# Kernel optimization log

Hardware: AMD Instinct MI355X
Metric: run time of the kernel (lower is better)

## Reference

```python
import jax, jax.numpy as jnp
import numpy as np

NUM_GROUPS = 32
EPS = 1e-6


def group_norm(x, gamma, beta):
    # x: [b, c, h, w]
    b, c, h, w = x.shape
    g = NUM_GROUPS
    xg = x.reshape(b, g, c // g, h, w)
    mean = jnp.mean(xg, axis=(2, 3, 4), keepdims=True)
    var = jnp.var(xg, axis=(2, 3, 4), keepdims=True)
    xg = (xg - mean) * jax.lax.rsqrt(var + EPS)
    x = xg.reshape(b, c, h, w)
    return x * gamma[None, :, None, None] + beta[None, :, None, None]


def conv1x1(x, w, bias):
    # x: [b, c_in, h, w], w: [c_out, c_in], bias: [c_out]
    return jnp.einsum('bihw,oi->bohw', x, w) + bias[None, :, None, None]


def setup_inputs() -> dict:
    key = jax.random.key(0)
    ks = jax.random.split(key, 10)
    c = 512
    b, h, w = 4, 64, 64
    scale = 1.0 / np.sqrt(c)
    inp = {
        'x': jax.random.normal(ks[0], (b, c, h, w), dtype=jnp.float32),
        'gn_gamma': jnp.ones((c,), dtype=jnp.float32),
        'gn_beta': jnp.zeros((c,), dtype=jnp.float32),
        'wq': jax.random.normal(ks[1], (c, c), dtype=jnp.float32) * scale,
        'bq': jnp.zeros((c,), dtype=jnp.float32),
        'wk': jax.random.normal(ks[2], (c, c), dtype=jnp.float32) * scale,
        'bk': jnp.zeros((c,), dtype=jnp.float32),
        'wv': jax.random.normal(ks[3], (c, c), dtype=jnp.float32) * scale,
        'bv': jnp.zeros((c,), dtype=jnp.float32),
        'wo': jax.random.normal(ks[4], (c, c), dtype=jnp.float32) * scale,
        'bo': jnp.zeros((c,), dtype=jnp.float32),
    }
    return inp


def reference(x, gn_gamma, gn_beta, wq, bq, wk, bk, wv, bv, wo, bo):
    b, c, h, w = x.shape
    h_ = group_norm(x, gn_gamma, gn_beta)
    q = conv1x1(h_, wq, bq)
    k = conv1x1(h_, wk, bk)
    v = conv1x1(h_, wv, bv)
    n = h * w
    q = q.reshape(b, c, n).transpose(0, 2, 1)  # [b, n, c]
    k = k.reshape(b, c, n)                      # [b, c, n]
    v = v.reshape(b, c, n).transpose(0, 2, 1)  # [b, n, c]
    sim = jnp.einsum('bqc,bck->bqk', q, k) * (c ** -0.5)  # [b, n, n]
    attn = jax.nn.softmax(sim, axis=-1)
    out = jnp.einsum('bqk,bkc->bqc', attn, v)  # [b, n, c]
    out = out.transpose(0, 2, 1).reshape(b, c, h, w)
    out = conv1x1(out, wo, bo)
    return x + out
```

## Files before the change

kernel.cpp:

```cpp
#include <hip/hip_runtime.h>


typedef __attribute__((ext_vector_type(8))) short bf16x8;
typedef __attribute__((ext_vector_type(4))) float f32x4;

#define MFMA16(a, b, c) __builtin_amdgcn_mfma_f32_16x16x32_bf16((a), (b), (c), 0, 0, 0)

#define B_   4
#define C_   512
#define N_   4096
#define SCALE 0.044194173824159216f
#define ESHIFT 12.0f

__device__ __forceinline__ unsigned short f2bf(float f) {
    union { float f; unsigned int u; } v; v.f = f;
    unsigned int r = (v.u + 0x7fffu + ((v.u >> 16) & 1u)) >> 16;
    return (unsigned short)r;
}
__device__ __forceinline__ float bf2f(unsigned short s) {
    union { unsigned int u; float f; } v; v.u = ((unsigned int)s) << 16;
    return v.f;
}

__device__ __forceinline__ void async16(const unsigned short* g, unsigned short* l) {
    __builtin_amdgcn_global_load_lds((const __attribute__((address_space(1))) unsigned int*)g,
                                     (__attribute__((address_space(3))) unsigned int*)l,
                                     16, 0, 0);
}

__global__ __launch_bounds__(256) void gn_partial(const float* __restrict__ x,
                                                  float* __restrict__ part) {
    int blk = blockIdx.x;
    int gid = blk >> 2, qtr = blk & 3;
    const float4* base = (const float4*)(x + (size_t)gid * 65536) + qtr * 4096;
    float s = 0.f, ss = 0.f;
    for (int i = threadIdx.x; i < 4096; i += 256) {
        float4 v = base[i];
        s  += v.x + v.y + v.z + v.w;
        ss += v.x * v.x + v.y * v.y + v.z * v.z + v.w * v.w;
    }
    __shared__ float red[512];
    int t = threadIdx.x;
    red[t] = s; red[256 + t] = ss;
    __syncthreads();
    for (int st = 128; st > 0; st >>= 1) {
        if (t < st) { red[t] += red[t + st]; red[256 + t] += red[256 + t + st]; }
        __syncthreads();
    }
    if (t == 0) { part[blk] = red[0]; part[512 + blk] = red[256]; }
}

__global__ __launch_bounds__(256) void gn_apply(const float* __restrict__ x,
                                                const float* __restrict__ gamma,
                                                const float* __restrict__ beta,
                                                const float* __restrict__ part,
                                                unsigned short* __restrict__ ht) {
    __shared__ float tile[64][65];
    __shared__ float mrs[4][2];
    int j0 = blockIdx.x * 64, c0 = blockIdx.y * 64, b = blockIdx.z;
    int t = threadIdx.x;
    if (t < 4) {
        int gid = b * 32 + (c0 >> 4) + t;
        float s = 0.f, ss = 0.f;
#pragma unroll
        for (int q = 0; q < 4; ++q) { s += part[gid * 4 + q]; ss += part[512 + gid * 4 + q]; }
        float mean = s * (1.f / 65536.f);
        float var  = ss * (1.f / 65536.f) - mean * mean;
        mrs[t][0] = mean;
        mrs[t][1] = rsqrtf(var + 1e-6f);
    }
    __syncthreads();
#pragma unroll
    for (int i = 0; i < 16; ++i) {
        int lid = i * 256 + t;
        int cl = lid >> 6, jl = lid & 63;
        int c = c0 + cl;
        float v = x[((size_t)b * C_ + c) * N_ + j0 + jl];
        tile[cl][jl] = (v - mrs[cl >> 4][0]) * mrs[cl >> 4][1] * gamma[c] + beta[c];
    }
    __syncthreads();
#pragma unroll
    for (int i = 0; i < 16; ++i) {
        int lid = i * 256 + t;
        int jl = lid >> 6, cl = lid & 63;
        ht[((size_t)b * N_ + j0 + jl) * C_ + c0 + cl] = f2bf(tile[cl][jl]);
    }
}

__global__ __launch_bounds__(256) void wconv(const float* __restrict__ wq,
                                             const float* __restrict__ wk,
                                             const float* __restrict__ wv,
                                             const float* __restrict__ wo,
                                             unsigned short* __restrict__ dst) {
    size_t i = (size_t)blockIdx.x * 256 + threadIdx.x;
    int m = (int)(i >> 18);
    size_t off = i & 262143;
    const float* src = (m == 0) ? wq : (m == 1) ? wk : (m == 2) ? wv : wo;
    dst[i] = f2bf(src[off]);
}

template <typename EPI>
__device__ __forceinline__ void gemm_core(const unsigned short* __restrict__ Abase,
                                          const unsigned short* __restrict__ Bbase,
                                          size_t lda, size_t ldb, int K, EPI epi) {
    __shared__ unsigned short hl[2][128 * 64];
    __shared__ unsigned short wl[2][128 * 64];
    int t = threadIdx.x;
    int wv = t >> 6, lane = t & 63, l15 = lane & 15, quad = lane >> 4;
    int wm = wv & 1, wn = wv >> 1;
    int srow = lane >> 3;
    int sch  = ((lane & 7) ^ srow) * 8;
    int xr = l15 & 7;
    f32x4 acc[4][4] = {};
#pragma unroll
    for (int i = 0; i < 4; ++i) {
        int seg = wv * 4 + i;
        size_t row = seg * 8 + srow;
        async16(&Abase[row * lda + sch], &hl[0][seg * 512]);
        async16(&Bbase[row * ldb + sch], &wl[0][seg * 512]);
    }
    int nk = K >> 6;
    for (int k = 0; k < nk; ++k) {
        int cur = k & 1;
        __builtin_amdgcn_s_waitcnt(0x3F70);
        __syncthreads();
        if (k + 1 < nk) {
            int k0 = (k + 1) << 6;
#pragma unroll
            for (int i = 0; i < 4; ++i) {
                int seg = wv * 4 + i;
                size_t row = seg * 8 + srow;
                async16(&Abase[row * lda + k0 + sch], &hl[cur ^ 1][seg * 512]);
                async16(&Bbase[row * ldb + k0 + sch], &wl[cur ^ 1][seg * 512]);
            }
        }
#pragma unroll
        for (int kk = 0; kk < 2; ++kk) {
            int sl = (((kk << 2) + quad) ^ xr) * 8;
            bf16x8 af[4], bfr[4];
#pragma unroll
            for (int mi = 0; mi < 4; ++mi)
                af[mi] = *(const bf16x8*)&hl[cur][(wm * 64 + mi * 16 + l15) * 64 + sl];
#pragma unroll
            for (int ni = 0; ni < 4; ++ni)
                bfr[ni] = *(const bf16x8*)&wl[cur][(wn * 64 + ni * 16 + l15) * 64 + sl];
#pragma unroll
            for (int mi = 0; mi < 4; ++mi)
#pragma unroll
                for (int ni = 0; ni < 4; ++ni)
                    acc[mi][ni] = MFMA16(af[mi], bfr[ni], acc[mi][ni]);
        }
    }
    epi(acc, wm, wn, l15, quad);
}

__global__ __launch_bounds__(256) void gemm_qkv(const unsigned short* __restrict__ Ht,
                                                const unsigned short* __restrict__ Wb,
                                                const float* __restrict__ bq,
                                                const float* __restrict__ bk,
                                                const float* __restrict__ bv,
                                                unsigned short* __restrict__ Qt,
                                                unsigned short* __restrict__ Kt,
                                                unsigned short* __restrict__ Vg) {
    int b = blockIdx.z, j0 = blockIdx.x * 128;
    int ct = blockIdx.y;
    int slab = ct >> 2, co0 = (ct & 3) * 128;
    const unsigned short* A = Ht + ((size_t)b * N_ + j0) * C_;
    const unsigned short* B = Wb + (size_t)slab * C_ * C_ + (size_t)co0 * C_;
    const float* bias = (slab == 0) ? bq : (slab == 1) ? bk : bv;
    unsigned short* outqk = (slab == 0) ? Qt : Kt;
    gemm_core(A, B, C_, C_, C_,
        [&](f32x4 (&acc)[4][4], int wm, int wn, int l15, int quad) {
        if (slab < 2) {
#pragma unroll
            for (int mi = 0; mi < 4; ++mi)
#pragma unroll
                for (int ni = 0; ni < 4; ++ni)
#pragma unroll
                    for (int r = 0; r < 4; ++r) {
                        int mrow = wm * 64 + mi * 16 + quad * 4 + r;
                        int ncol = wn * 64 + ni * 16 + l15;
                        outqk[((size_t)b * N_ + j0 + mrow) * C_ + co0 + ncol] =
                            f2bf(acc[mi][ni][r] + bias[co0 + ncol]);
                    }
        } else {
#pragma unroll
            for (int mi = 0; mi < 4; ++mi)
#pragma unroll
                for (int ni = 0; ni < 4; ++ni) {
                    int ncol = wn * 64 + ni * 16 + l15;
                    float bb = bias[co0 + ncol];
                    ushort4 pk;
                    pk.x = f2bf(acc[mi][ni][0] + bb);
                    pk.y = f2bf(acc[mi][ni][1] + bb);
                    pk.z = f2bf(acc[mi][ni][2] + bb);
                    pk.w = f2bf(acc[mi][ni][3] + bb);
                    int jb = j0 + wm * 64 + mi * 16 + quad * 4;
                    *(ushort4*)&Vg[((size_t)b * C_ + co0 + ncol) * N_ + jb] = pk;
                }
        }
    });
}

__global__ __launch_bounds__(256) void gemm_qk_exp(const unsigned short* __restrict__ Qt,
                                                   const unsigned short* __restrict__ Kt,
                                                   unsigned short* __restrict__ P,
                                                   float* __restrict__ psum) {
    int b = blockIdx.z, j0 = blockIdx.x * 128, ktile = blockIdx.y;
    int kc0 = ktile * 128;
    const unsigned short* A = Qt + ((size_t)b * N_ + j0) * C_;
    const unsigned short* B = Kt + ((size_t)b * N_ + kc0) * C_;
    gemm_core(A, B, C_, C_, C_,
        [&](f32x4 (&acc)[4][4], int wm, int wn, int l15, int quad) {
        float rs[4][4];
#pragma unroll
        for (int mi = 0; mi < 4; ++mi)
#pragma unroll
            for (int r = 0; r < 4; ++r) rs[mi][r] = 0.f;
#pragma unroll
        for (int mi = 0; mi < 4; ++mi)
#pragma unroll
            for (int ni = 0; ni < 4; ++ni)
#pragma unroll
                for (int r = 0; r < 4; ++r) {
                    int mrow = wm * 64 + mi * 16 + quad * 4 + r;
                    int ncol = wn * 64 + ni * 16 + l15;
                    float p = __expf(acc[mi][ni][r] * SCALE - ESHIFT);
                    rs[mi][r] += p;
                    P[((size_t)b * N_ + j0 + mrow) * N_ + kc0 + ncol] = f2bf(p);
                }
#pragma unroll
        for (int mi = 0; mi < 4; ++mi)
#pragma unroll
            for (int r = 0; r < 4; ++r) {
                float v = rs[mi][r];
                v += __shfl_xor(v, 1);
                v += __shfl_xor(v, 2);
                v += __shfl_xor(v, 4);
                v += __shfl_xor(v, 8);
                if (l15 == 0)
                    psum[(size_t)(wn * 32 + ktile) * 16384 +
                         (size_t)b * N_ + j0 + wm * 64 + mi * 16 + quad * 4 + r] = v;
            }
    });
}

__global__ __launch_bounds__(256) void gemm_pv(const unsigned short* __restrict__ P,
                                               const unsigned short* __restrict__ Vg,
                                               const float* __restrict__ psum,
                                               unsigned short* __restrict__ ao) {
    __shared__ float linv[128];
    int flat = blockIdx.x;
    int xcd = flat & 7, rr = flat >> 3;
    int ct = rr & 3, g = (rr >> 2) * 8 + xcd;
    int b = g & 3, qtile = g >> 2;
    int j0 = qtile * 128, co0 = ct * 128;
    int t = threadIdx.x;
    if (t < 128) {
        size_t q = (size_t)b * N_ + j0 + t;
        float s = 0.f;
#pragma unroll
        for (int i = 0; i < 64; ++i) s += psum[(size_t)i * 16384 + q];
        linv[t] = 1.f / s;
    }
    const unsigned short* A = P + ((size_t)b * N_ + j0) * N_;
    const unsigned short* B = Vg + ((size_t)b * C_ + co0) * N_;
    gemm_core(A, B, N_, N_, N_,
        [&](f32x4 (&acc)[4][4], int wm, int wn, int l15, int quad) {
#pragma unroll
        for (int mi = 0; mi < 4; ++mi)
#pragma unroll
            for (int ni = 0; ni < 4; ++ni)
#pragma unroll
                for (int r = 0; r < 4; ++r) {
                    int mrow = wm * 64 + mi * 16 + quad * 4 + r;
                    int ncol = wn * 64 + ni * 16 + l15;
                    ao[((size_t)b * N_ + j0 + mrow) * C_ + co0 + ncol] =
                        f2bf(acc[mi][ni][r] * linv[mrow]);
                }
    });
}

__global__ __launch_bounds__(256) void gemm_resid(const unsigned short* __restrict__ AObf,
                                                  const unsigned short* __restrict__ Wo,
                                                  const float* __restrict__ bo,
                                                  const float* __restrict__ xres,
                                                  float* __restrict__ out) {
    int b = blockIdx.z, j0 = blockIdx.x * 128, co0 = blockIdx.y * 128;
    const unsigned short* A = AObf + ((size_t)b * N_ + j0) * C_;
    const unsigned short* B = Wo + (size_t)co0 * C_;
    gemm_core(A, B, C_, C_, C_,
        [&](f32x4 (&acc)[4][4], int wm, int wn, int l15, int quad) {
#pragma unroll
        for (int mi = 0; mi < 4; ++mi)
#pragma unroll
            for (int ni = 0; ni < 4; ++ni) {
                int ncol = wn * 64 + ni * 16 + l15;
                int jb = j0 + wm * 64 + mi * 16 + quad * 4;
                size_t o = ((size_t)b * C_ + co0 + ncol) * N_ + jb;
                float bb = bo[co0 + ncol];
                float4 xr = *(const float4*)&xres[o];
                float4 ov;
                ov.x = acc[mi][ni][0] + bb + xr.x;
                ov.y = acc[mi][ni][1] + bb + xr.y;
                ov.z = acc[mi][ni][2] + bb + xr.z;
                ov.w = acc[mi][ni][3] + bb + xr.w;
                *(float4*)&out[o] = ov;
            }
    });
}

__global__ __launch_bounds__(256, 1) void flash_attn(const unsigned short* __restrict__ Qt,
                                                     const unsigned short* __restrict__ Kt,
                                                     const unsigned short* __restrict__ Vg,
                                                     unsigned short* __restrict__ part,
                                                     float* __restrict__ lbuf,
                                                     int nsplit) {
    extern __shared__ unsigned short smem[];
    unsigned short* Kl = smem;
    unsigned short* Vl = smem + 32768;
    unsigned short* Pl = smem + 65536;

    int flat = blockIdx.x;
    int qblk, b, s;
    if (nsplit == 2) { s = flat & 1; b = (flat >> 1) & 3; qblk = flat >> 3; }
    else             { s = 0;        b = flat & 3;        qblk = flat >> 2; }
    int q0 = qblk * 128;
    int t = threadIdx.x, w = t >> 6, lane = t & 63, l15 = lane & 15, quad = lane >> 4;
    int klen = N_ / nsplit, kbeg = s * klen, nkt = klen / 32;
    int xr = l15 & 7;

    const unsigned short* Kbase = Kt + (size_t)b * N_ * C_;
    const unsigned short* Vbase = Vg + (size_t)b * C_ * N_;

    bf16x8 qa[2][16];
#pragma unroll
    for (int u = 0; u < 2; ++u) {
        const unsigned short* qb =
            Qt + ((size_t)b * N_ + q0 + w * 32 + u * 16 + l15) * C_ + quad * 8;
#pragma unroll
        for (int ck = 0; ck < 16; ++ck) qa[u][ck] = *(const bf16x8*)(qb + ck * 32);
    }

    f32x4 o[2][32] = {};
    float lrow[2][4] = {};

    {
        int k0 = kbeg;
#pragma unroll
        for (int i = 0; i < 8; ++i) {
            int r = w * 8 + i;
            async16(Kbase + (size_t)(k0 + r) * C_ + ((lane ^ (r & 7)) * 8), Kl + r * 512);
        }
#pragma unroll
        for (int i = 0; i < 8; ++i) {
            int idx = w * 8 + i, kc = idx >> 3, cb = idx & 7;
            async16(Vbase + (size_t)(cb * 64 + lane) * N_ + k0 + kc * 8,
                    Vl + (kc * 512 + cb * 64) * 8);
        }
    }

    for (int kt = 0; kt < nkt; ++kt) {
        int cur = kt & 1, nxt = cur ^ 1;
        __builtin_amdgcn_s_waitcnt(0x3F70);
        __syncthreads();
        if (kt + 1 < nkt) {
            int k0 = kbeg + (kt + 1) * 32;
#pragma unroll
            for (int i = 0; i < 8; ++i) {
                int r = w * 8 + i;
                async16(Kbase + (size_t)(k0 + r) * C_ + ((lane ^ (r & 7)) * 8),
                        Kl + nxt * 16384 + r * 512);
            }
#pragma unroll
            for (int i = 0; i < 8; ++i) {
                int idx = w * 8 + i, kc = idx >> 3, cb = idx & 7;
                async16(Vbase + (size_t)(cb * 64 + lane) * N_ + k0 + kc * 8,
                        Vl + nxt * 16384 + (kc * 512 + cb * 64) * 8);
            }
        }
        const unsigned short* Kc = Kl + cur * 16384;
        f32x4 s00 = {}, s01 = {}, s10 = {}, s11 = {};
#pragma unroll
        for (int ck = 0; ck < 16; ++ck) {
            int slot = (ck * 4 + quad) ^ xr;
            bf16x8 b0 = *(const bf16x8*)&Kc[l15 * 512 + slot * 8];
            bf16x8 b1 = *(const bf16x8*)&Kc[(16 + l15) * 512 + slot * 8];
            s00 = MFMA16(qa[0][ck], b0, s00);
            s10 = MFMA16(qa[1][ck], b0, s10);
            s01 = MFMA16(qa[0][ck], b1, s01);
            s11 = MFMA16(qa[1][ck], b1, s11);
        }
        unsigned short* pb = &Pl[w * 1152];
#pragma unroll
        for (int r = 0; r < 4; ++r) {
            float p00 = __expf(s00[r] * SCALE - ESHIFT);
            float p01 = __expf(s01[r] * SCALE - ESHIFT);
            float p10 = __expf(s10[r] * SCALE - ESHIFT);
            float p11 = __expf(s11[r] * SCALE - ESHIFT);
            lrow[0][r] += p00 + p01;
            lrow[1][r] += p10 + p11;
            int row0 = (quad * 4 + r) * 36;
            int row1 = (16 + quad * 4 + r) * 36;
            pb[row0 + l15]      = f2bf(p00);
            pb[row0 + 16 + l15] = f2bf(p01);
            pb[row1 + l15]      = f2bf(p10);
            pb[row1 + 16 + l15] = f2bf(p11);
        }
        __builtin_amdgcn_s_waitcnt(0xC07F);
        bf16x8 pa0 = *(const bf16x8*)&Pl[w * 1152 + l15 * 36 + quad * 8];
        bf16x8 pa1 = *(const bf16x8*)&Pl[w * 1152 + (16 + l15) * 36 + quad * 8];
        const unsigned short* Vc = Vl + cur * 16384;
#pragma unroll
        for (int cf = 0; cf < 32; ++cf) {
            bf16x8 vb = *(const bf16x8*)&Vc[(quad * 512 + cf * 16 + l15) * 8];
            o[0][cf] = MFMA16(pa0, vb, o[0][cf]);
            o[1][cf] = MFMA16(pa1, vb, o[1][cf]);
        }
    }
#pragma unroll
    for (int u = 0; u < 2; ++u)
#pragma unroll
        for (int r = 0; r < 4; ++r) {
            float l = lrow[u][r];
            l += __shfl_xor(l, 1);
            l += __shfl_xor(l, 2);
            l += __shfl_xor(l, 4);
            l += __shfl_xor(l, 8);
            lrow[u][r] = l;
        }
    size_t pbase = (size_t)(s * B_ + b) * N_;
#pragma unroll
    for (int u = 0; u < 2; ++u)
#pragma unroll
        for (int cf = 0; cf < 32; ++cf)
#pragma unroll
            for (int r = 0; r < 4; ++r) {
                int q = q0 + w * 32 + u * 16 + quad * 4 + r;
                part[(pbase + q) * C_ + cf * 16 + l15] = f2bf(o[u][cf][r]);
            }
    if (l15 == 0) {
#pragma unroll
        for (int u = 0; u < 2; ++u)
#pragma unroll
            for (int r = 0; r < 4; ++r) {
                int q = q0 + w * 32 + u * 16 + quad * 4 + r;
                lbuf[pbase + q] = lrow[u][r];
            }
    }
}

__global__ __launch_bounds__(256) void attn_combine(const unsigned short* __restrict__ part,
                                                    const float* __restrict__ lbuf,
                                                    unsigned short* __restrict__ ao,
                                                    int nsplit) {
    size_t idx = (size_t)blockIdx.x * 256 + threadIdx.x;
    int cu = (int)(idx & 63);
    size_t row = idx >> 6;
    float l = lbuf[row];
    union { uint4 v; unsigned short u[8]; } p1, p2, outv;
    p1.v = *(const uint4*)&part[row * C_ + cu * 8];
    if (nsplit == 2) {
        l += lbuf[(size_t)B_ * N_ + row];
        p2.v = *(const uint4*)&part[((size_t)B_ * N_ + row) * C_ + cu * 8];
    } else {
        p2.v = make_uint4(0, 0, 0, 0);
    }
    float inv = 1.f / l;
#pragma unroll
    for (int j = 0; j < 8; ++j)
        outv.u[j] = f2bf((bf2f(p1.u[j]) + bf2f(p2.u[j])) * inv);
    *(uint4*)&ao[row * C_ + cu * 8] = outv.v;
}

extern "C" void kernel_launch(void* const* d_in, const int* in_sizes, int n_in,
                              void* d_out, int out_size, void* d_ws, size_t ws_size,
                              hipStream_t stream) {
    const float* x   = (const float*)d_in[0];
    const float* gam = (const float*)d_in[1];
    const float* bet = (const float*)d_in[2];
    const float* wq  = (const float*)d_in[3];
    const float* bq  = (const float*)d_in[4];
    const float* wk  = (const float*)d_in[5];
    const float* bk  = (const float*)d_in[6];
    const float* wv  = (const float*)d_in[7];
    const float* bv  = (const float*)d_in[8];
    const float* wo  = (const float*)d_in[9];
    const float* bo  = (const float*)d_in[10];
    float* out = (float*)d_out;

    char* ws = (char*)d_ws;
    const size_t SZH = (size_t)B_ * N_ * C_ * 2;
    const size_t OFF_HT = 4096;
    const size_t OFF_QT = OFF_HT + SZH;
    const size_t OFF_KT = OFF_QT + SZH;
    const size_t OFF_VG = OFF_KT + SZH;
    const size_t OFF_WB = OFF_VG + SZH;
    const size_t OFF_X  = OFF_WB + 2097152;
    float*          part0 = (float*)ws;
    unsigned short* Ht    = (unsigned short*)(ws + OFF_HT);
    unsigned short* Qt    = (unsigned short*)(ws + OFF_QT);
    unsigned short* Kt    = (unsigned short*)(ws + OFF_KT);
    unsigned short* Vg    = (unsigned short*)(ws + OFF_VG);
    unsigned short* Wb    = (unsigned short*)(ws + OFF_WB);
    unsigned short* AObf  = Ht;

    const size_t SZPSUM = 64ull * 16384 * 4;
    const size_t SZP    = (size_t)B_ * N_ * N_ * 2;
    float*          psum = (float*)(ws + OFF_X);
    unsigned short* P    = (unsigned short*)(ws + OFF_X + SZPSUM);
    size_t needA = OFF_X + SZPSUM + SZP;

    float*          lbuf = (float*)(ws + OFF_X);
    unsigned short* partb = (unsigned short*)(ws + OFF_X + 262144);
    size_t needB2 = OFF_X + 262144 + 2 * SZH;

    gn_partial<<<512, 256, 0, stream>>>(x, part0);
    gn_apply<<<dim3(64, 8, B_), 256, 0, stream>>>(x, gam, bet, part0, Ht);
    wconv<<<4096, 256, 0, stream>>>(wq, wk, wv, wo, Wb);
    gemm_qkv<<<dim3(32, 12, B_), 256, 0, stream>>>(Ht, Wb, bq, bk, bv, Qt, Kt, Vg);

    if (ws_size >= needA) {
        gemm_qk_exp<<<dim3(32, 32, B_), 256, 0, stream>>>(Qt, Kt, P, psum);
        gemm_pv<<<512, 256, 0, stream>>>(P, Vg, psum, AObf);
    } else {
        int nsplit = (ws_size >= needB2) ? 2 : 1;
        const int FLASH_LDS = 140288;
        (void)hipFuncSetAttribute((const void*)flash_attn,
                                  hipFuncAttributeMaxDynamicSharedMemorySize, FLASH_LDS);
        flash_attn<<<dim3(32 * B_ * nsplit), 256, FLASH_LDS, stream>>>(Qt, Kt, Vg, partb, lbuf, nsplit);
        attn_combine<<<4096, 256, 0, stream>>>(partb, lbuf, AObf, nsplit);
    }
    gemm_resid<<<dim3(32, 4, B_), 256, 0, stream>>>(AObf, Wb + 786432, bo, x, out);
}
```

Baseline: 370.3 us.

## Rewrite QK-exp GEMM with 256x256 tiles and a 4-stage async LDS pipeline

The score GEMM moves from the shared 128x128 gemm_core to a dedicated kernel. Each 512-thread block computes a 256x256 tile through a 4-deep ring of swizzled LDS buffers filled by async global-to-LDS copies, with barrier-split MFMA phases and raised wave priority around the MFMAs. The larger tile cuts redundant Q/K reloads, and the deeper pipeline is meant to hide load latency. The exp, bf16 store of P and partial row sums keep the same 64-partial psum layout. The cost is 128KB of dynamic LDS per block, which limits occupancy to one block per CU, plus more register pressure from the 8x4 accumulators.

Result: faster. 352.4 us (-4.8%).

```diff
diff --git a/kernel.cpp b/kernel.cpp
--- a/kernel.cpp
+++ b/kernel.cpp
@@ -202,47 +202,123 @@
     });
 }
 
-__global__ __launch_bounds__(256) void gemm_qk_exp(const unsigned short* __restrict__ Qt,
-                                                   const unsigned short* __restrict__ Kt,
-                                                   unsigned short* __restrict__ P,
-                                                   float* __restrict__ psum) {
-    int b = blockIdx.z, j0 = blockIdx.x * 128, ktile = blockIdx.y;
-    int kc0 = ktile * 128;
-    const unsigned short* A = Qt + ((size_t)b * N_ + j0) * C_;
-    const unsigned short* B = Kt + ((size_t)b * N_ + kc0) * C_;
-    gemm_core(A, B, C_, C_, C_,
-        [&](f32x4 (&acc)[4][4], int wm, int wn, int l15, int quad) {
-        float rs[4][4];
+__global__ __launch_bounds__(512, 2) void gemm_qk_exp(const unsigned short* __restrict__ Qt,
+                                                      const unsigned short* __restrict__ Kt,
+                                                      unsigned short* __restrict__ P,
+                                                      float* __restrict__ psum) {
+    extern __shared__ unsigned short sm[];
+    int b = blockIdx.z, j0 = blockIdx.x * 256, ky = blockIdx.y;
+    int kc0 = ky * 256;
+    const unsigned short* A  = Qt + ((size_t)b * N_ + j0) * C_;
+    const unsigned short* Bm = Kt + ((size_t)b * N_ + kc0) * C_;
+
+    int t = threadIdx.x;
+    int w = t >> 6, lane = t & 63, l15 = lane & 15, quad = lane >> 4;
+    int wm = w >> 2, wn = w & 3;
+    int srow = lane >> 2;
+    int sch  = (((lane & 3) ^ ((lane >> 3) & 3))) * 8;
+    int slotq = (quad ^ ((l15 >> 1) & 3)) * 8;
+
+    f32x4 acc[8][4] = {};
+
+    const int NT = 16;
+#pragma unroll
+    for (int tt = 0; tt < 3; ++tt) {
+        unsigned short* dst = sm + (tt << 14);
+        size_t k0 = (size_t)tt << 5;
+#pragma unroll
+        for (int i = 0; i < 2; ++i) {
+            int seg = w * 2 + i;
+            size_t row = (size_t)seg * 16 + srow;
+            async16(&A [row * C_ + k0 + sch], dst + seg * 512);
+            async16(&Bm[row * C_ + k0 + sch], dst + 8192 + seg * 512);
+        }
+    }
+    __builtin_amdgcn_s_waitcnt(0x3F78);
+    __builtin_amdgcn_s_barrier();
+
+    for (int tt = 0; tt < NT; ++tt) {
+        const unsigned short* bp = sm + ((tt & 3) << 14);
+        unsigned short* stg = sm + (((tt + 3) & 3) << 14);
+        const bool dostage = (tt + 3 < NT);
+        size_t k0n = (size_t)(tt + 3) << 5;
+        bf16x8 bfr[4], af[4];
+#pragma unroll
+        for (int ni = 0; ni < 4; ++ni)
+            bfr[ni] = *(const bf16x8*)&bp[8192 + (wn * 64 + ni * 16 + l15) * 32 + slotq];
 #pragma unroll
         for (int mi = 0; mi < 4; ++mi)
-#pragma unroll
-            for (int r = 0; r < 4; ++r) rs[mi][r] = 0.f;
+            af[mi] = *(const bf16x8*)&bp[(wm * 128 + mi * 16 + l15) * 32 + slotq];
+        if (dostage) {
+#pragma unroll
+            for (int i = 0; i < 2; ++i) {
+                int seg = w * 2 + i;
+                size_t row = (size_t)seg * 16 + srow;
+                async16(&A[row * C_ + k0n + sch], stg + seg * 512);
+            }
+        }
+        __builtin_amdgcn_s_barrier();
+        __builtin_amdgcn_s_setprio(1);
 #pragma unroll
         for (int mi = 0; mi < 4; ++mi)
 #pragma unroll
             for (int ni = 0; ni < 4; ++ni)
-#pragma unroll
-                for (int r = 0; r < 4; ++r) {
-                    int mrow = wm * 64 + mi * 16 + quad * 4 + r;
-                    int ncol = wn * 64 + ni * 16 + l15;
-                    float p = __expf(acc[mi][ni][r] * SCALE - ESHIFT);
-                    rs[mi][r] += p;
-                    P[((size_t)b * N_ + j0 + mrow) * N_ + kc0 + ncol] = f2bf(p);
-                }
+                acc[mi][ni] = MFMA16(af[mi], bfr[ni], acc[mi][ni]);
+        __builtin_amdgcn_s_setprio(0);
+        __builtin_amdgcn_s_barrier();
 #pragma unroll
         for (int mi = 0; mi < 4; ++mi)
+            af[mi] = *(const bf16x8*)&bp[(wm * 128 + (mi + 4) * 16 + l15) * 32 + slotq];
+        if (dostage) {
+#pragma unroll
+            for (int i = 0; i < 2; ++i) {
+                int seg = w * 2 + i;
+                size_t row = (size_t)seg * 16 + srow;
+                async16(&Bm[row * C_ + k0n + sch], stg + 8192 + seg * 512);
+            }
+        }
+        __builtin_amdgcn_s_barrier();
+        __builtin_amdgcn_s_setprio(1);
+#pragma unroll
+        for (int mi = 0; mi < 4; ++mi)
+#pragma unroll
+            for (int ni = 0; ni < 4; ++ni)
+                acc[4 + mi][ni] = MFMA16(af[mi], bfr[ni], acc[4 + mi][ni]);
+        __builtin_amdgcn_s_setprio(0);
+        if (tt + 1 < NT) {
+            if (tt < NT - 3)       __builtin_amdgcn_s_waitcnt(0x3F78);
+            else if (tt == NT - 3) __builtin_amdgcn_s_waitcnt(0x3F74);
+            else                   __builtin_amdgcn_s_waitcnt(0x3F70);
+            __builtin_amdgcn_s_barrier();
+        }
+    }
+
+#pragma unroll
+    for (int mi = 0; mi < 8; ++mi) {
+        float rs[4] = {0.f, 0.f, 0.f, 0.f};
+#pragma unroll
+        for (int ni = 0; ni < 4; ++ni) {
+            int ncol = kc0 + wn * 64 + ni * 16 + l15;
 #pragma unroll
             for (int r = 0; r < 4; ++r) {
-                float v = rs[mi][r];
-                v += __shfl_xor(v, 1);
-                v += __shfl_xor(v, 2);
-                v += __shfl_xor(v, 4);
-                v += __shfl_xor(v, 8);
-                if (l15 == 0)
-                    psum[(size_t)(wn * 32 + ktile) * 16384 +
-                         (size_t)b * N_ + j0 + wm * 64 + mi * 16 + quad * 4 + r] = v;
-            }
-    });
+                int mrow = j0 + wm * 128 + mi * 16 + quad * 4 + r;
+                float p = __expf(acc[mi][ni][r] * SCALE - ESHIFT);
+                rs[r] += p;
+                P[((size_t)b * N_ + mrow) * N_ + ncol] = f2bf(p);
+            }
+        }
+#pragma unroll
+        for (int r = 0; r < 4; ++r) {
+            float v = rs[r];
+            v += __shfl_xor(v, 1);
+            v += __shfl_xor(v, 2);
+            v += __shfl_xor(v, 4);
+            v += __shfl_xor(v, 8);
+            if (l15 == 0)
+                psum[(size_t)(wn * 16 + ky) * 16384 +
+                     (size_t)b * N_ + j0 + wm * 128 + mi * 16 + quad * 4 + r] = v;
+        }
+    }
 }
 
 __global__ __launch_bounds__(256) void gemm_pv(const unsigned short* __restrict__ P,
@@ -521,7 +597,10 @@
     gemm_qkv<<<dim3(32, 12, B_), 256, 0, stream>>>(Ht, Wb, bq, bk, bv, Qt, Kt, Vg);
 
     if (ws_size >= needA) {
-        gemm_qk_exp<<<dim3(32, 32, B_), 256, 0, stream>>>(Qt, Kt, P, psum);
+        const int QK_LDS = 131072;
+        (void)hipFuncSetAttribute((const void*)gemm_qk_exp,
+                                  hipFuncAttributeMaxDynamicSharedMemorySize, QK_LDS);
+        gemm_qk_exp<<<dim3(16, 16, B_), 512, QK_LDS, stream>>>(Qt, Kt, P, psum);
         gemm_pv<<<512, 256, 0, stream>>>(P, Vg, psum, AObf);
     } else {
         int nsplit = (ws_size >= needB2) ? 2 : 1;
```
